# Kernel tuning notes

Measured on AMD Instinct MI355X. Metric: run time of the kernel, lower is better.

Reference implementation:

```python
import jax, jax.numpy as jnp
import numpy as np

FEATURE_DIM = 1024
HEADS = 16
HEAD_DIM = FEATURE_DIM // HEADS


def setup_inputs() -> dict:
    key = jax.random.key(0)
    ks = jax.random.split(key, 9)
    B, C, T = 4, FEATURE_DIM, 4096
    s = 1.0 / np.sqrt(C)
    inp = {
        "x": jax.random.normal(ks[0], (B, C, T), dtype=jnp.float32),
        "Wq": jax.random.uniform(ks[1], (C, C), jnp.float32, -s, s),
        "bq": jax.random.uniform(ks[2], (C,), jnp.float32, -s, s),
        "Wk": jax.random.uniform(ks[3], (C, C), jnp.float32, -s, s),
        "bk": jax.random.uniform(ks[4], (C,), jnp.float32, -s, s),
        "Wv": jax.random.uniform(ks[5], (C, C), jnp.float32, -s, s),
        "bv": jax.random.uniform(ks[6], (C,), jnp.float32, -s, s),
        "Wo": jax.random.uniform(ks[7], (C, C), jnp.float32, -s, s),
        "bo": jax.random.uniform(ks[8], (C,), jnp.float32, -s, s),
    }
    return inp


def reference(x, Wq, bq, Wk, bk, Wv, bv, Wo, bo):
    B, C, T = x.shape
    H, D = HEADS, HEAD_DIM
    xt = jnp.transpose(x, (0, 2, 1))  # [B, T, C]
    # torch Linear: y = x @ W.T + b
    q = jax.nn.elu(xt @ Wq.T + bq).reshape(B, T, H, D) + 1.0
    k = jax.nn.elu(xt @ Wk.T + bk).reshape(B, T, H, D) + 1.0
    v = (xt @ Wv.T + bv).reshape(B, T, H, D)
    kv = jnp.einsum('bthd,bthe->bhde', k, v)      # [B, H, D, D]
    z = jnp.einsum('bthd,bhd->bth', q, k.sum(axis=1))  # [B, T, H]
    num = jnp.einsum('bthd,bhde->bthe', q, kv)    # [B, T, H, D]
    out = num / (z[..., None] + 1e-6)
    out = out.reshape(B, T, C)
    out = out @ Wo.T + bo  # dropout is identity in eval mode
    return jnp.transpose(out + xt, (0, 2, 1))  # [B, C, T]
```

## Files before the change

kernel.cpp:

```cpp
#include <hip/hip_runtime.h>
#include <hip/hip_bf16.h>
#include <cmath>

typedef unsigned short u16;
typedef unsigned int   u32;

#define BB 4
#define CC 1024
#define TT 4096
#define HH 16
#define DD 64

using bf16x8 = __attribute__((ext_vector_type(8))) __bf16;
using f32x4  = __attribute__((ext_vector_type(4))) float;

union FragU { bf16x8 v; u16 u[8]; };

__device__ __forceinline__ float bf2f(u16 u) {
    union { u32 i; float f; } v; v.i = ((u32)u) << 16; return v.f;
}
__device__ __forceinline__ u16 f2bf(float f) {
    union { float f; u32 i; } v; v.f = f;
    u32 x = v.i;
    return (u16)((x + 0x7fffu + ((x >> 16) & 1u)) >> 16);
}

__device__ __forceinline__ void gl_lds16(const u16* g, u16* l) {
    __builtin_amdgcn_global_load_lds(
        (const __attribute__((address_space(1))) void*)g,
        (__attribute__((address_space(3))) void*)l, 16, 0, 0);
}

__global__ __launch_bounds__(256) void prep_kernel(
    const float* __restrict__ x,
    const float* __restrict__ Wq, const float* __restrict__ Wk,
    const float* __restrict__ Wv, const float* __restrict__ Wo,
    u16* __restrict__ xt, u16* __restrict__ Wcat, u16* __restrict__ Wob,
    float* __restrict__ kvz)
{
    __shared__ u16 tile[64 * 258];
    const int id  = blockIdx.x;
    const int tid = threadIdx.x;

    if (id < 1024) {
        const int t0 = (id & 63) * 64;
        const int c0 = ((id >> 6) & 3) * 256;
        const int b  = id >> 8;
        const float* xb  = x  + (size_t)b * CC * TT;
        u16*         xtb = xt + (size_t)b * TT * CC;
        const int tcol = tid & 63;
        const int rw   = tid >> 6;
        #pragma unroll 8
        for (int p = 0; p < 64; ++p) {
            const int cr = p * 4 + rw;
            tile[tcol * 258 + cr] = f2bf(xb[(size_t)(c0 + cr) * TT + t0 + tcol]);
        }
        __syncthreads();
        const int cp = tid & 127;
        const int th = tid >> 7;
        #pragma unroll 8
        for (int q = 0; q < 32; ++q) {
            const int tr = q * 2 + th;
            const u32 v = *reinterpret_cast<const u32*>(&tile[tr * 258 + cp * 2]);
            *reinterpret_cast<u32*>(&xtb[(size_t)(t0 + tr) * CC + c0 + cp * 2]) = v;
        }
    } else if (id < 5120) {
        const int id2  = id - 1024;
        const int wsel = id2 >> 10;
        const int i    = ((id2 & 1023) * 256 + tid) * 4;
        const float* src = (wsel == 0) ? Wq : (wsel == 1) ? Wk : (wsel == 2) ? Wv : Wo;
        u16* dst = (wsel < 3) ? (Wcat + (size_t)wsel * CC * CC) : Wob;
        const float4 v = *reinterpret_cast<const float4*>(src + i);
        ushort4 o;
        o.x = f2bf(v.x); o.y = f2bf(v.y); o.z = f2bf(v.z); o.w = f2bf(v.w);
        *reinterpret_cast<ushort4*>(dst + i) = o;
    } else {
        const int idx = ((id - 5120) * 256 + tid) * 4;
        *reinterpret_cast<float4*>(&kvz[idx]) = (float4){0.f, 0.f, 0.f, 0.f};
    }
}

__global__ __launch_bounds__(256, 2) void kvfuse_kernel(
    const u16* __restrict__ A, const u16* __restrict__ Wk,
    const u16* __restrict__ Wv, const float* __restrict__ bk,
    const float* __restrict__ bv, float* __restrict__ kv,
    float* __restrict__ ksum)
{
    __shared__ __align__(16) char smem[65536];
    u16* As  = (u16*)smem;
    u16* WKs = (u16*)(smem + 16384);
    u16* WVs = (u16*)(smem + 32768);

    const int tid  = threadIdx.x;
    const int w    = tid >> 6;
    const int lane = tid & 63;
    const int wm = w >> 1, wn = w & 1;
    const int quad = lane >> 4, l16 = lane & 15;
    const int n0 = blockIdx.x * 128;
    const int m0 = blockIdx.y * 128;

    const int srow = lane >> 3;
    const int scol = ((lane & 7) ^ srow) * 8;

    f32x4 ak[4][4], av[4][4];
    #pragma unroll
    for (int i = 0; i < 4; ++i)
        #pragma unroll
        for (int j = 0; j < 4; ++j) { ak[i][j] = (f32x4)0.0f; av[i][j] = (f32x4)0.0f; }

    for (int k0 = 0; k0 < CC; k0 += 64) {
        __syncthreads();
        #pragma unroll
        for (int s = 0; s < 4; ++s) {
            gl_lds16(A  + (size_t)(m0 + 32 * w + 8 * s + srow) * CC + k0 + scol,
                     &As [(32 * w + 8 * s) * 64]);
            gl_lds16(Wk + (size_t)(n0 + 32 * w + 8 * s + srow) * CC + k0 + scol,
                     &WKs[(32 * w + 8 * s) * 64]);
            gl_lds16(Wv + (size_t)(n0 + 32 * w + 8 * s + srow) * CC + k0 + scol,
                     &WVs[(32 * w + 8 * s) * 64]);
        }
        __syncthreads();

        #pragma unroll
        for (int sub = 0; sub < 2; ++sub) {
            const int pg = (((sub << 2) | quad) ^ (l16 & 7)) * 8;
            bf16x8 af[4], bk4[4], bv4[4];
            #pragma unroll
            for (int i = 0; i < 4; ++i) {
                af[i]  = *reinterpret_cast<const bf16x8*>(&As [(wm * 64 + i * 16 + l16) * 64 + pg]);
                bk4[i] = *reinterpret_cast<const bf16x8*>(&WKs[(wn * 64 + i * 16 + l16) * 64 + pg]);
                bv4[i] = *reinterpret_cast<const bf16x8*>(&WVs[(wn * 64 + i * 16 + l16) * 64 + pg]);
            }
            #pragma unroll
            for (int i = 0; i < 4; ++i)
                #pragma unroll
                for (int j = 0; j < 4; ++j) {
                    ak[i][j] = __builtin_amdgcn_mfma_f32_16x16x32_bf16(af[i], bk4[j], ak[i][j], 0, 0, 0);
                    av[i][j] = __builtin_amdgcn_mfma_f32_16x16x32_bf16(af[i], bv4[j], av[i][j], 0, 0, 0);
                }
        }
    }

    __syncthreads();
    u16* Kl = (u16*)smem;
    u16* Vl = (u16*)(smem + 32768);

    float bkk[4], bvv[4];
    #pragma unroll
    for (int j = 0; j < 4; ++j) {
        bkk[j] = bk[n0 + wn * 64 + j * 16 + l16];
        bvv[j] = bv[n0 + wn * 64 + j * 16 + l16];
    }
    #pragma unroll
    for (int i = 0; i < 4; ++i) {
        const int t4 = wm * 64 + i * 16 + quad * 4;
        #pragma unroll
        for (int j = 0; j < 4; ++j) {
            const int c    = wn * 64 + j * 16 + l16;
            const int toff = t4 ^ ((c & 15) * 8);
            ushort4 oK, oV;
            #pragma unroll
            for (int r = 0; r < 4; ++r) {
                float vK = ak[i][j][r] + bkk[j];
                vK = (vK > 0.0f) ? (vK + 1.0f) : __expf(vK);
                ((u16*)&oK)[r] = f2bf(vK);
                ((u16*)&oV)[r] = f2bf(av[i][j][r] + bvv[j]);
            }
            *reinterpret_cast<ushort4*>(&Kl[c * 128 + toff]) = oK;
            *reinterpret_cast<ushort4*>(&Vl[c * 128 + toff]) = oV;
        }
    }
    __syncthreads();

    const int hh    = w >> 1;
    const int dbase = (w & 1) * 32;
    const int b     = m0 >> 12;
    const int bh    = b * HH + blockIdx.x * 2 + hh;

    FragU ones;
    #pragma unroll
    for (int j = 0; j < 8; ++j) ones.u[j] = (l16 == 0) ? 0x3F80u : 0u;

    f32x4 ckv[2][4], cks[2];
    #pragma unroll
    for (int s = 0; s < 2; ++s) {
        cks[s] = (f32x4)0.0f;
        #pragma unroll
        for (int e4 = 0; e4 < 4; ++e4) ckv[s][e4] = (f32x4)0.0f;
    }

    #pragma unroll
    for (int kt = 0; kt < 4; ++kt) {
        const int tg = kt * 32 + quad * 8;
        #pragma unroll
        for (int s = 0; s < 2; ++s) {
            const int ca = hh * 64 + dbase + s * 16 + l16;
            const bf16x8 af = *reinterpret_cast<const bf16x8*>(
                &Kl[ca * 128 + (tg ^ (l16 * 8))]);
            #pragma unroll
            for (int e4 = 0; e4 < 4; ++e4) {
                const int cb = hh * 64 + e4 * 16 + l16;
                const bf16x8 bfv = *reinterpret_cast<const bf16x8*>(
                    &Vl[cb * 128 + (tg ^ (l16 * 8))]);
                ckv[s][e4] = __builtin_amdgcn_mfma_f32_16x16x32_bf16(af, bfv, ckv[s][e4], 0, 0, 0);
            }
            cks[s] = __builtin_amdgcn_mfma_f32_16x16x32_bf16(af, ones.v, cks[s], 0, 0, 0);
        }
    }

    float* kvb = kv + (size_t)bh * DD * DD;
    #pragma unroll
    for (int s = 0; s < 2; ++s)
        #pragma unroll
        for (int e4 = 0; e4 < 4; ++e4)
            #pragma unroll
            for (int r = 0; r < 4; ++r)
                atomicAdd(&kvb[(dbase + s * 16 + quad * 4 + r) * DD + e4 * 16 + l16],
                          ckv[s][e4][r]);
    if (l16 == 0) {
        #pragma unroll
        for (int s = 0; s < 2; ++s)
            #pragma unroll
            for (int r = 0; r < 4; ++r)
                atomicAdd(&ksum[bh * DD + dbase + s * 16 + quad * 4 + r], cks[s][r]);
    }
}

__global__ __launch_bounds__(256, 2) void qattn_kernel(
    const u16* __restrict__ A, const u16* __restrict__ Wq,
    const float* __restrict__ bq, const float* __restrict__ kv,
    const float* __restrict__ ksum, u16* __restrict__ attnO)
{
    __shared__ __align__(16) char smem[32768];
    u16* As = (u16*)smem;
    u16* Ws = (u16*)(smem + 16384);

    const int tid  = threadIdx.x;
    const int w    = tid >> 6;
    const int lane = tid & 63;
    const int wm = w >> 1, wn = w & 1;
    const int quad = lane >> 4, l16 = lane & 15;
    const int l7 = l16 & 7;
    const int n0 = blockIdx.x * 128;
    const int m0 = blockIdx.y * 128;

    const int srow = lane >> 3;
    const int scol = ((lane & 7) ^ srow) * 8;

    f32x4 acc[4][4];
    #pragma unroll
    for (int i = 0; i < 4; ++i)
        #pragma unroll
        for (int j = 0; j < 4; ++j) acc[i][j] = (f32x4)0.0f;

    for (int k0 = 0; k0 < CC; k0 += 64) {
        __syncthreads();
        #pragma unroll
        for (int s = 0; s < 4; ++s) {
            gl_lds16(A  + (size_t)(m0 + 32 * w + 8 * s + srow) * CC + k0 + scol,
                     &As[(32 * w + 8 * s) * 64]);
            gl_lds16(Wq + (size_t)(n0 + 32 * w + 8 * s + srow) * CC + k0 + scol,
                     &Ws[(32 * w + 8 * s) * 64]);
        }
        __syncthreads();

        #pragma unroll
        for (int sub = 0; sub < 2; ++sub) {
            const int pg = (((sub << 2) | quad) ^ l7) * 8;
            bf16x8 af[4], bfr[4];
            #pragma unroll
            for (int i = 0; i < 4; ++i) {
                af[i]  = *reinterpret_cast<const bf16x8*>(&As[(wm * 64 + i * 16 + l16) * 64 + pg]);
                bfr[i] = *reinterpret_cast<const bf16x8*>(&Ws[(wn * 64 + i * 16 + l16) * 64 + pg]);
            }
            #pragma unroll
            for (int i = 0; i < 4; ++i)
                #pragma unroll
                for (int j = 0; j < 4; ++j)
                    acc[i][j] = __builtin_amdgcn_mfma_f32_16x16x32_bf16(af[i], bfr[j], acc[i][j], 0, 0, 0);
        }
    }

    __syncthreads();
    u16* Qt = (u16*)smem;
    float bqq[4];
    #pragma unroll
    for (int j = 0; j < 4; ++j) bqq[j] = bq[n0 + wn * 64 + j * 16 + l16];
    #pragma unroll
    for (int i = 0; i < 4; ++i) {
        #pragma unroll
        for (int j = 0; j < 4; ++j) {
            const int c = wn * 64 + j * 16 + l16;
            #pragma unroll
            for (int r = 0; r < 4; ++r) {
                const int t = wm * 64 + i * 16 + quad * 4 + r;
                float v = acc[i][j][r] + bqq[j];
                v = (v > 0.0f) ? (v + 1.0f) : __expf(v);
                Qt[t * 128 + (c ^ ((t & 7) * 8))] = f2bf(v);
            }
        }
    }
    __syncthreads();

    const int hh = w >> 1, th = w & 1;
    const int b  = m0 >> 12;
    const int bh = b * HH + blockIdx.x * 2 + hh;
    const float* kvh = kv + (size_t)bh * DD * DD;

    FragU bf[4][2], zb[2];
    #pragma unroll
    for (int ck = 0; ck < 2; ++ck) {
        #pragma unroll
        for (int nt = 0; nt < 4; ++nt)
            #pragma unroll
            for (int j = 0; j < 8; ++j)
                bf[nt][ck].u[j] = f2bf(kvh[(ck * 32 + quad * 8 + j) * DD + nt * 16 + l16]);
        #pragma unroll
        for (int j = 0; j < 8; ++j)
            zb[ck].u[j] = (l16 == 0) ? f2bf(ksum[bh * DD + ck * 32 + quad * 8 + j]) : 0u;
    }

    f32x4 a2[4][4], za[4];
    #pragma unroll
    for (int i = 0; i < 4; ++i) {
        za[i] = (f32x4)0.0f;
        #pragma unroll
        for (int j = 0; j < 4; ++j) a2[i][j] = (f32x4)0.0f;
    }

    #pragma unroll
    for (int i = 0; i < 4; ++i) {
        const int trow = th * 64 + i * 16 + l16;
        #pragma unroll
        for (int ck = 0; ck < 2; ++ck) {
            const bf16x8 af = *reinterpret_cast<const bf16x8*>(
                &Qt[trow * 128 + (((hh * 8 + ck * 4 + quad) ^ l7) * 8)]);
            #pragma unroll
            for (int nt = 0; nt < 4; ++nt)
                a2[i][nt] = __builtin_amdgcn_mfma_f32_16x16x32_bf16(af, bf[nt][ck].v, a2[i][nt], 0, 0, 0);
            za[i] = __builtin_amdgcn_mfma_f32_16x16x32_bf16(af, zb[ck].v, za[i], 0, 0, 0);
        }
    }

    #pragma unroll
    for (int i = 0; i < 4; ++i) {
        float inv[4];
        #pragma unroll
        for (int r = 0; r < 4; ++r) {
            const float zv = __shfl(za[i][r], lane & 48);
            inv[r] = 1.0f / (zv + 1e-6f);
        }
        #pragma unroll
        for (int nt = 0; nt < 4; ++nt) {
            #pragma unroll
            for (int r = 0; r < 4; ++r) {
                const size_t row = (size_t)(m0 + th * 64 + i * 16 + quad * 4 + r);
                const int    col = n0 + hh * 64 + nt * 16 + l16;
                attnO[row * CC + col] = f2bf(a2[i][nt][r] * inv[r]);
            }
        }
    }
}

template <int MODE>
__global__ __launch_bounds__(256, 2) void gemm_kernel(
    const u16* __restrict__ A, const u16* __restrict__ W,
    const float* __restrict__ b0, const float* __restrict__ b1,
    const float* __restrict__ b2, u16* __restrict__ Ybf,
    float* __restrict__ Yf, const float* __restrict__ xres,
    int M, int N, int K)
{
    __shared__ char smem[34048];
    u16* As = (u16*)smem;
    u16* Ws = (u16*)(smem + 16384);

    const int tid  = threadIdx.x;
    const int w    = tid >> 6;
    const int lane = tid & 63;
    const int wm = w >> 1, wn = w & 1;
    const int quad = lane >> 4, l16 = lane & 15;
    const int m0 = blockIdx.y * 128;
    const int n0 = blockIdx.x * 128;

    const int srow = lane >> 3;
    const int scol = ((lane & 7) ^ srow) * 8;

    f32x4 acc[4][4];
    #pragma unroll
    for (int i = 0; i < 4; ++i)
        #pragma unroll
        for (int j = 0; j < 4; ++j) acc[i][j] = (f32x4)0.0f;

    for (int k0 = 0; k0 < K; k0 += 64) {
        __syncthreads();
        #pragma unroll
        for (int s = 0; s < 4; ++s)
            gl_lds16(A + (size_t)(m0 + 32 * w + 8 * s + srow) * K + k0 + scol,
                     &As[(32 * w + 8 * s) * 64]);
        #pragma unroll
        for (int s = 0; s < 4; ++s)
            gl_lds16(W + (size_t)(n0 + 32 * w + 8 * s + srow) * K + k0 + scol,
                     &Ws[(32 * w + 8 * s) * 64]);
        __syncthreads();

        #pragma unroll
        for (int sub = 0; sub < 2; ++sub) {
            const int pg = (((sub << 2) | quad) ^ (l16 & 7)) * 8;
            bf16x8 af[4], bfr[4];
            #pragma unroll
            for (int i = 0; i < 4; ++i) {
                af[i]  = *reinterpret_cast<const bf16x8*>(&As[(wm * 64 + i * 16 + l16) * 64 + pg]);
                bfr[i] = *reinterpret_cast<const bf16x8*>(&Ws[(wn * 64 + i * 16 + l16) * 64 + pg]);
            }
            #pragma unroll
            for (int i = 0; i < 4; ++i)
                #pragma unroll
                for (int j = 0; j < 4; ++j)
                    acc[i][j] = __builtin_amdgcn_mfma_f32_16x16x32_bf16(af[i], bfr[j], acc[i][j], 0, 0, 0);
        }
    }

    if (MODE == 2) {
        float* Cs = (float*)smem;
        const int b     = m0 / TT;
        const int tbase = m0 - b * TT;
        const int cl    = lane >> 4;
        #pragma unroll
        for (int hh = 0; hh < 2; ++hh) {
            __syncthreads();
            if (wm == hh) {
                #pragma unroll
                for (int i = 0; i < 4; ++i)
                    #pragma unroll
                    for (int j = 0; j < 4; ++j)
                        #pragma unroll
                        for (int r = 0; r < 4; ++r)
                            Cs[(i * 16 + quad * 4 + r) * 133 + wn * 64 + j * 16 + l16] = acc[i][j][r];
            }
            __syncthreads();
            #pragma unroll
            for (int p = 0; p < 8; ++p) {
                const int col = p * 16 + w * 4 + cl;
                const int tl  = l16 * 4;
                float4 v;
                v.x = Cs[(tl + 0) * 133 + col];
                v.y = Cs[(tl + 1) * 133 + col];
                v.z = Cs[(tl + 2) * 133 + col];
                v.w = Cs[(tl + 3) * 133 + col];
                const float bv = b0[n0 + col];
                const size_t base = ((size_t)b * CC + n0 + col) * TT + tbase + hh * 64 + tl;
                const float4 rx = *reinterpret_cast<const float4*>(&xres[base]);
                v.x += bv + rx.x; v.y += bv + rx.y;
                v.z += bv + rx.z; v.w += bv + rx.w;
                *reinterpret_cast<float4*>(&Yf[base]) = v;
            }
        }
    }
}

extern "C" void kernel_launch(void* const* d_in, const int* in_sizes, int n_in,
                              void* d_out, int out_size, void* d_ws, size_t ws_size,
                              hipStream_t stream)
{
    const float* x  = (const float*)d_in[0];
    const float* Wq = (const float*)d_in[1];
    const float* bq = (const float*)d_in[2];
    const float* Wk = (const float*)d_in[3];
    const float* bk = (const float*)d_in[4];
    const float* Wv = (const float*)d_in[5];
    const float* bv = (const float*)d_in[6];
    const float* Wo = (const float*)d_in[7];
    const float* bo = (const float*)d_in[8];
    float* out = (float*)d_out;

    const int M = BB * TT;
    const size_t BUF  = (size_t)BB * TT * CC * sizeof(u16);
    const size_t WBUF = (size_t)CC * CC * sizeof(u16);

    char* ws = (char*)d_ws;
    u16* xt   = (u16*)(ws);
    u16* Qb   = (u16*)(ws + BUF);
    u16* Wcat = (u16*)(ws + 4 * BUF);
    u16* Wob  = (u16*)(ws + 4 * BUF + 3 * WBUF);
    float* kvbuf = (float*)(ws + 4 * BUF + 4 * WBUF);
    float* ksumb = kvbuf + (size_t)BB * HH * DD * DD;

    prep_kernel<<<5380, 256, 0, stream>>>(x, Wq, Wk, Wv, Wo, xt, Wcat, Wob, kvbuf);

    kvfuse_kernel<<<dim3(CC / 128, M / 128), 256, 0, stream>>>(
        xt, Wcat + (size_t)CC * CC, Wcat + 2 * (size_t)CC * CC, bk, bv, kvbuf, ksumb);

    qattn_kernel<<<dim3(CC / 128, M / 128), 256, 0, stream>>>(
        xt, Wcat, bq, kvbuf, ksumb, Qb);

    gemm_kernel<2><<<dim3(CC / 128, M / 128), 256, 0, stream>>>(
        Qb, Wob, bo, nullptr, nullptr, nullptr, out, x, M, CC, CC);
}
```

Before: 337.6 us.

## Swizzle block order per XCD and halve kvfuse epilogue LDS staging

Launches all three GEMM-style kernels on a 1D grid and remaps block IDs so blocks sharing an XCD process the same row tile across all column tiles, improving L2 reuse of activations. The kvfuse epilogue now stages K/V into LDS in two 64-token halves instead of one 128-token pass. This shrinks shared memory from 64KB to 48KB, potentially raising occupancy, at the cost of extra barriers and serialized epilogue phases.

New measurement: 322.3 us. 4.5% less time.

```diff
diff --git a/kernel.cpp b/kernel.cpp
--- a/kernel.cpp
+++ b/kernel.cpp
@@ -86,7 +86,7 @@
     const float* __restrict__ bv, float* __restrict__ kv,
     float* __restrict__ ksum)
 {
-    __shared__ __align__(16) char smem[65536];
+    __shared__ __align__(16) char smem[49152];
     u16* As  = (u16*)smem;
     u16* WKs = (u16*)(smem + 16384);
     u16* WVs = (u16*)(smem + 32768);
@@ -96,8 +96,11 @@
     const int lane = tid & 63;
     const int wm = w >> 1, wn = w & 1;
     const int quad = lane >> 4, l16 = lane & 15;
-    const int n0 = blockIdx.x * 128;
-    const int m0 = blockIdx.y * 128;
+
+    const int bid = blockIdx.x;
+    const int sw  = (bid & 7) * 128 + (bid >> 3);
+    const int n0  = (sw & 7) * 128;
+    const int m0  = (sw >> 3) * 128;
 
     const int srow = lane >> 3;
     const int scol = ((lane & 7) ^ srow) * 8;
@@ -141,9 +144,8 @@
         }
     }
 
-    __syncthreads();
     u16* Kl = (u16*)smem;
-    u16* Vl = (u16*)(smem + 32768);
+    u16* Vl = (u16*)(smem + 16384);
 
     float bkk[4], bvv[4];
     #pragma unroll
@@ -151,31 +153,11 @@
         bkk[j] = bk[n0 + wn * 64 + j * 16 + l16];
         bvv[j] = bv[n0 + wn * 64 + j * 16 + l16];
     }
-    #pragma unroll
-    for (int i = 0; i < 4; ++i) {
-        const int t4 = wm * 64 + i * 16 + quad * 4;
-        #pragma unroll
-        for (int j = 0; j < 4; ++j) {
-            const int c    = wn * 64 + j * 16 + l16;
-            const int toff = t4 ^ ((c & 15) * 8);
-            ushort4 oK, oV;
-            #pragma unroll
-            for (int r = 0; r < 4; ++r) {
-                float vK = ak[i][j][r] + bkk[j];
-                vK = (vK > 0.0f) ? (vK + 1.0f) : __expf(vK);
-                ((u16*)&oK)[r] = f2bf(vK);
-                ((u16*)&oV)[r] = f2bf(av[i][j][r] + bvv[j]);
-            }
-            *reinterpret_cast<ushort4*>(&Kl[c * 128 + toff]) = oK;
-            *reinterpret_cast<ushort4*>(&Vl[c * 128 + toff]) = oV;
-        }
-    }
-    __syncthreads();
 
     const int hh    = w >> 1;
     const int dbase = (w & 1) * 32;
     const int b     = m0 >> 12;
-    const int bh    = b * HH + blockIdx.x * 2 + hh;
+    const int bh    = b * HH + (sw & 7) * 2 + hh;
 
     FragU ones;
     #pragma unroll
@@ -190,21 +172,47 @@
     }
 
     #pragma unroll
-    for (int kt = 0; kt < 4; ++kt) {
-        const int tg = kt * 32 + quad * 8;
-        #pragma unroll
-        for (int s = 0; s < 2; ++s) {
-            const int ca = hh * 64 + dbase + s * 16 + l16;
-            const bf16x8 af = *reinterpret_cast<const bf16x8*>(
-                &Kl[ca * 128 + (tg ^ (l16 * 8))]);
-            #pragma unroll
-            for (int e4 = 0; e4 < 4; ++e4) {
-                const int cb = hh * 64 + e4 * 16 + l16;
-                const bf16x8 bfv = *reinterpret_cast<const bf16x8*>(
-                    &Vl[cb * 128 + (tg ^ (l16 * 8))]);
-                ckv[s][e4] = __builtin_amdgcn_mfma_f32_16x16x32_bf16(af, bfv, ckv[s][e4], 0, 0, 0);
-            }
-            cks[s] = __builtin_amdgcn_mfma_f32_16x16x32_bf16(af, ones.v, cks[s], 0, 0, 0);
+    for (int h = 0; h < 2; ++h) {
+        __syncthreads();
+        if (wm == h) {
+            #pragma unroll
+            for (int i = 0; i < 4; ++i) {
+                const int t6 = i * 16 + quad * 4;
+                #pragma unroll
+                for (int j = 0; j < 4; ++j) {
+                    const int c    = wn * 64 + j * 16 + l16;
+                    const int toff = t6 ^ ((c & 7) * 8);
+                    ushort4 oK, oV;
+                    #pragma unroll
+                    for (int r = 0; r < 4; ++r) {
+                        float vK = ak[i][j][r] + bkk[j];
+                        vK = (vK > 0.0f) ? (vK + 1.0f) : __expf(vK);
+                        ((u16*)&oK)[r] = f2bf(vK);
+                        ((u16*)&oV)[r] = f2bf(av[i][j][r] + bvv[j]);
+                    }
+                    *reinterpret_cast<ushort4*>(&Kl[c * 64 + toff]) = oK;
+                    *reinterpret_cast<ushort4*>(&Vl[c * 64 + toff]) = oV;
+                }
+            }
+        }
+        __syncthreads();
+        #pragma unroll
+        for (int kt = 0; kt < 2; ++kt) {
+            const int tg = kt * 32 + quad * 8;
+            #pragma unroll
+            for (int s = 0; s < 2; ++s) {
+                const int ca = hh * 64 + dbase + s * 16 + l16;
+                const bf16x8 af = *reinterpret_cast<const bf16x8*>(
+                    &Kl[ca * 64 + (tg ^ ((ca & 7) * 8))]);
+                #pragma unroll
+                for (int e4 = 0; e4 < 4; ++e4) {
+                    const int cb = hh * 64 + e4 * 16 + l16;
+                    const bf16x8 bfv = *reinterpret_cast<const bf16x8*>(
+                        &Vl[cb * 64 + (tg ^ ((cb & 7) * 8))]);
+                    ckv[s][e4] = __builtin_amdgcn_mfma_f32_16x16x32_bf16(af, bfv, ckv[s][e4], 0, 0, 0);
+                }
+                cks[s] = __builtin_amdgcn_mfma_f32_16x16x32_bf16(af, ones.v, cks[s], 0, 0, 0);
+            }
         }
     }
 
@@ -241,8 +249,11 @@
     const int wm = w >> 1, wn = w & 1;
     const int quad = lane >> 4, l16 = lane & 15;
     const int l7 = l16 & 7;
-    const int n0 = blockIdx.x * 128;
-    const int m0 = blockIdx.y * 128;
+
+    const int bid = blockIdx.x;
+    const int sw  = (bid & 7) * 128 + (bid >> 3);
+    const int n0  = (sw & 7) * 128;
+    const int m0  = (sw >> 3) * 128;
 
     const int srow = lane >> 3;
     const int scol = ((lane & 7) ^ srow) * 8;
@@ -304,7 +315,7 @@
 
     const int hh = w >> 1, th = w & 1;
     const int b  = m0 >> 12;
-    const int bh = b * HH + blockIdx.x * 2 + hh;
+    const int bh = b * HH + (sw & 7) * 2 + hh;
     const float* kvh = kv + (size_t)bh * DD * DD;
 
     FragU bf[4][2], zb[2];
@@ -379,8 +390,11 @@
     const int lane = tid & 63;
     const int wm = w >> 1, wn = w & 1;
     const int quad = lane >> 4, l16 = lane & 15;
-    const int m0 = blockIdx.y * 128;
-    const int n0 = blockIdx.x * 128;
+
+    const int bid = blockIdx.x;
+    const int sw  = (bid & 7) * 128 + (bid >> 3);
+    const int n0  = (sw & 7) * 128;
+    const int m0  = (sw >> 3) * 128;
 
     const int srow = lane >> 3;
     const int scol = ((lane & 7) ^ srow) * 8;
@@ -487,12 +501,12 @@
 
     prep_kernel<<<5380, 256, 0, stream>>>(x, Wq, Wk, Wv, Wo, xt, Wcat, Wob, kvbuf);
 
-    kvfuse_kernel<<<dim3(CC / 128, M / 128), 256, 0, stream>>>(
+    kvfuse_kernel<<<1024, 256, 0, stream>>>(
         xt, Wcat + (size_t)CC * CC, Wcat + 2 * (size_t)CC * CC, bk, bv, kvbuf, ksumb);
 
-    qattn_kernel<<<dim3(CC / 128, M / 128), 256, 0, stream>>>(
+    qattn_kernel<<<1024, 256, 0, stream>>>(
         xt, Wcat, bq, kvbuf, ksumb, Qb);
 
-    gemm_kernel<2><<<dim3(CC / 128, M / 128), 256, 0, stream>>>(
+    gemm_kernel<2><<<1024, 256, 0, stream>>>(
         Qb, Wob, bo, nullptr, nullptr, nullptr, out, x, M, CC, CC);
 }
```
